# Optimization experiments

Hardware: AMD Instinct MI355X
Metric: run time of the kernel (lower is better)

## Reference

```python
import jax, jax.numpy as jnp
import numpy as np
from jax import lax

G = 16            # graphs in batch
N0 = 2048         # total nodes (128 per graph)
IN_CH = 64
HID = 128
KS = (103, 83)    # ceil(0.8*128), ceil(0.8*103): per-graph nodes kept by each ASAPooling
NEG_SLOPE = 0.2   # ASAPooling leaky_relu slope


def _masked_col_max(M, x, chunk=4):
    # out[i, c] = max_{j : M[j, i]} x[j, c]  (scatter-max over incoming edges), feature-chunked
    N, C = x.shape
    xr = x.T.reshape(C // chunk, chunk, N)
    @jax.checkpoint
    def f(xc):  # [chunk, N_j]
        v = jnp.where(M[None, :, :], xc[:, :, None], -1e30)  # [chunk, j, i]
        return v.max(axis=1)
    return lax.map(f, xr).reshape(C, N).T


def _graph_conv(x, A, w_rel, b_rel, w_root):
    # PyG GraphConv(aggr='mean'): lin_rel(mean_j w_ji * x_j) + lin_root(x); A[src,dst]
    deg = jnp.maximum((A != 0).sum(0).astype(x.dtype), 1.0)  # incoming edge count
    agg = (A.T @ x) / deg[:, None]
    return agg @ w_rel.T + b_rel + x @ w_root.T


def _gpool(x):  # global_mean_pool over equal-sized contiguous graphs
    return x.reshape(G, -1, x.shape[-1]).mean(axis=1)


def _asap_pool(x, A, k, lin_w, lin_b, att_w, att_b, le1_w, le1_b, le2_w, le3_w, le3_b):
    N, C = x.shape
    one = jnp.asarray(1.0, x.dtype)
    A = jnp.where(jnp.eye(N, dtype=bool), one, A)  # add_remaining_self_loops(fill=1)
    M = A != 0
    Mf = M.astype(x.dtype)
    # master query: max over incoming neighbors, then Linear
    q = _masked_col_max(M, x) @ lin_w.T + lin_b                     # [N, C]
    a_q, a_x = att_w[:C], att_w[C:]                                 # att(cat([x_q_i, x_j]))
    logits = jax.nn.leaky_relu((x @ a_x)[:, None] + (q @ a_q)[None, :] + att_b, NEG_SLOPE)  # [j, i]
    S = jnp.where(M, jax.nn.softmax(jnp.where(M, logits, -1e30), axis=0), 0.0)
    x_new = S.T @ x                                                  # cluster reps
    # fitness = sigmoid(LEConv(x_new)): lin3(x_i) + sum_j (lin1(x_j) - lin2(x_i)) over edges
    deg = Mf.sum(0)
    a = x_new @ le1_w + le1_b
    b = x_new @ le2_w
    fitness = jax.nn.sigmoid(Mf.T @ a - deg * b + x_new @ le3_w + le3_b)  # [N]
    n_cur = N // G
    idx = lax.top_k(fitness.reshape(G, n_cur), k)[1]                 # per-graph top-k
    perm = (idx + jnp.arange(G)[:, None] * n_cur).reshape(-1)        # [G*k], grouped by graph
    x_out = x_new[perm] * fitness[perm][:, None]
    S_sel = S[:, perm]                                               # [N, K]
    A2 = S_sel.T @ (A @ S_sel)                                       # S^T A S coarsening
    A2 = jnp.where(jnp.eye(G * k, dtype=bool), one, A2)              # fill_diag(1)
    return x_out, A2


def _forward(x, edge_index, c0_wrel, c0_brel, c0_wroot, cw_rel, cb_rel, cw_root,
             p_lin_w, p_lin_b, p_att_w, p_att_b, p_le1_w, p_le1_b, p_le2_w,
             p_le3_w, p_le3_b, lin1_w, lin1_b, lin2_w, lin2_b):
    A = jnp.zeros((N0, N0), x.dtype).at[edge_index[0], edge_index[1]].add(1.0)
    h = jax.nn.relu(_graph_conv(x, A, c0_wrel, c0_brel, c0_wroot))
    xs = [_gpool(h)]
    p = 0
    for i in range(4):  # num_layers - 1 convs
        h = jax.nn.relu(_graph_conv(h, A, cw_rel[i], cb_rel[i], cw_root[i]))
        xs.append(_gpool(h))
        if i % 2 == 0 and i < 3:
            h, A = _asap_pool(h, A, KS[p], p_lin_w[p], p_lin_b[p], p_att_w[p], p_att_b[p],
                              p_le1_w[p], p_le1_b[p], p_le2_w[p], p_le3_w[p], p_le3_b[p])
            p += 1
    j = jnp.concatenate(xs, axis=-1)                                  # JK 'cat': [G, 5*HID]
    z = jax.nn.relu(j @ lin1_w.T + lin1_b)                            # dropout: eval mode (identity)
    z = z @ lin2_w.T + lin2_b
    return jax.nn.log_softmax(z, axis=-1)


def setup_inputs() -> dict:
    key = jax.random.key(0)
    rng = np.random.default_rng(0)
    n, deg = N0 // G, 16
    sc = rng.random((G, n, n))
    sc[:, np.arange(n), np.arange(n)] = -1.0  # no self loops
    dst = np.argsort(-sc, axis=-1)[:, :, :deg]  # 16 distinct neighbors per node
    src = np.broadcast_to(np.arange(n)[None, :, None], dst.shape)
    off = (np.arange(G) * n)[:, None, None]
    edge_index = jnp.asarray(np.stack([(src + off).ravel(), (dst + off).ravel()]), dtype=jnp.int32)
    ks = jax.random.split(key, 16)
    def lin(k, shape, fan_in):
        return jax.random.normal(k, shape, jnp.float32) / np.sqrt(fan_in)
    return dict(
        x=jax.random.normal(ks[0], (N0, IN_CH), jnp.float32),
        edge_index=edge_index,
        c0_wrel=lin(ks[1], (HID, IN_CH), IN_CH),
        c0_brel=jnp.zeros((HID,), jnp.float32),
        c0_wroot=lin(ks[2], (HID, IN_CH), IN_CH),
        cw_rel=lin(ks[3], (4, HID, HID), HID),
        cb_rel=jnp.zeros((4, HID), jnp.float32),
        cw_root=lin(ks[4], (4, HID, HID), HID),
        p_lin_w=lin(ks[5], (2, HID, HID), HID),
        p_lin_b=jnp.zeros((2, HID), jnp.float32),
        p_att_w=lin(ks[6], (2, 2 * HID), 2 * HID),
        p_att_b=jnp.zeros((2,), jnp.float32),
        p_le1_w=lin(ks[7], (2, HID), HID),
        p_le1_b=jnp.zeros((2,), jnp.float32),
        p_le2_w=lin(ks[8], (2, HID), HID),
        p_le3_w=lin(ks[9], (2, HID), HID),
        p_le3_b=jnp.zeros((2,), jnp.float32),
        lin1_w=lin(ks[10], (HID, 5 * HID), 5 * HID),
        lin1_b=jnp.zeros((HID,), jnp.float32),
        lin2_w=lin(ks[11], (2, HID), HID),
        lin2_b=jnp.zeros((2,), jnp.float32),
    )


def reference(x, edge_index, c0_wrel, c0_brel, c0_wroot, cw_rel, cb_rel, cw_root,
              p_lin_w, p_lin_b, p_att_w, p_att_b, p_le1_w, p_le1_b, p_le2_w,
              p_le3_w, p_le3_b, lin1_w, lin1_b, lin2_w, lin2_b):
    return _forward(x, edge_index, c0_wrel, c0_brel, c0_wroot, cw_rel, cb_rel, cw_root,
                    p_lin_w, p_lin_b, p_att_w, p_att_b, p_le1_w, p_le1_b, p_le2_w,
                    p_le3_w, p_le3_b, lin1_w, lin1_b, lin2_w, lin2_b)
```

## Files before the change

kernel.cpp:

```cpp
#include <hip/hip_runtime.h>

#define NEG_SLOPE 0.2f
typedef unsigned int u32;

__global__ __launch_bounds__(256) void k_build(const int* __restrict__ ei,
                                               u32* __restrict__ Mb,
                                               u32* __restrict__ Rb, int E)
{
    int e = blockIdx.x * 256 + threadIdx.x;
    if (e >= E) return;
    int s = ei[e], d = ei[E + e];
    int g = s >> 7, ls = s & 127, ld = d & 127;
    atomicOr(&Mb[(g * 128 + ld) * 4 + (ls >> 5)], 1u << (ls & 31));
    atomicOr(&Rb[(g * 128 + ls) * 4 + (ld >> 5)], 1u << (ld & 31));
}

__global__ __launch_bounds__(128) void k_prep(
    const float* __restrict__ lin_w, const float* __restrict__ lin_b,
    const float* __restrict__ att_w,
    float* __restrict__ v_out, float* __restrict__ c0_out)
{
    const int p = blockIdx.x;
    const float* lw = lin_w + p * 16384;
    const float* lb = lin_b + p * 128;
    const float* aw = att_w + p * 256;
    const int c = threadIdx.x;
    float s = 0.f;
    for (int c2 = 0; c2 < 128; ++c2) s += aw[c2] * lw[c2 * 128 + c];
    v_out[p * 128 + c] = s;
    if (c < 64) {
        float s0 = aw[c] * lb[c] + aw[c + 64] * lb[c + 64];
        for (int off = 32; off; off >>= 1) s0 += __shfl_xor(s0, off);
        if (c == 0) c0_out[p] = s0;
    }
}

__global__ __launch_bounds__(512) void k_agg_mask(
    const float* __restrict__ h, const u32* __restrict__ Mb,
    float* __restrict__ agg, int n, int Cin)
{
    const int g = blockIdx.x;
    const int q4 = Cin >> 2;
    int idx = blockIdx.y * 512 + threadIdx.x;
    if (idx >= n * q4) return;
    int j = idx / q4, c4 = (idx - j * q4) << 2;
    const u32* m = Mb + (g * 128 + j) * 4;
    u32 m0 = m[0], m1 = m[1], m2 = m[2], m3 = m[3];
    float dv = fmaxf((float)(__popc(m0) + __popc(m1) + __popc(m2) + __popc(m3)), 1.0f);
    const float* hg = h + (size_t)g * n * Cin + c4;
    float sx = 0.f, sy = 0.f, sz = 0.f, sw = 0.f;
    u32 wds[4] = { m0, m1, m2, m3 };
    #pragma unroll
    for (int ww = 0; ww < 4; ++ww) {
        u32 u = wds[ww];
        while (u) {
            int i = (ww << 5) + __ffs(u) - 1; u &= u - 1u;
            float4 hv = *(const float4*)(hg + (size_t)i * Cin);
            sx += hv.x; sy += hv.y; sz += hv.z; sw += hv.w;
        }
    }
    float4 o; o.x = sx / dv; o.y = sy / dv; o.z = sz / dv; o.w = sw / dv;
    *(float4*)(agg + ((size_t)g * n + j) * Cin + c4) = o;
}

__global__ __launch_bounds__(512) void k_agg_dense(
    const float* __restrict__ h, const float* __restrict__ AT,
    const u32* __restrict__ Mb, float* __restrict__ agg, int n)
{
    const int C = 128;
    const int g = blockIdx.x;
    int idx = blockIdx.y * 512 + threadIdx.x;
    if (idx >= n * 32) return;
    int j = idx >> 5, c4 = (idx & 31) << 2;
    const u32* m = Mb + (g * 128 + j) * 4;
    float dv = fmaxf((float)(__popc(m[0]) + __popc(m[1]) + __popc(m[2]) + __popc(m[3])), 1.0f);
    const float* Aj = AT + ((size_t)g * n + j) * n;
    const float* hg = h + (size_t)g * n * C + c4;
    float sx = 0.f, sy = 0.f, sz = 0.f, sw = 0.f;
    for (int i = 0; i < n; ++i) {
        float a = Aj[i];
        float4 hv = *(const float4*)(hg + (size_t)i * C);
        sx += a * hv.x; sy += a * hv.y; sz += a * hv.z; sw += a * hv.w;
    }
    float4 o; o.x = sx / dv; o.y = sy / dv; o.z = sz / dv; o.w = sw / dv;
    *(float4*)(agg + ((size_t)g * n + j) * C + c4) = o;
}

template<int CIN>
__global__ __launch_bounds__(512) void k_out(
    const float* __restrict__ h, const float* __restrict__ agg,
    const float* __restrict__ wrel, const float* __restrict__ brel,
    const float* __restrict__ wroot,
    float* __restrict__ h_out, float* __restrict__ xs,
    int n)
{
    constexpr int L = CIN >> 1;
    constexpr int G = 512 / L;
    constexpr int HALF = L >> 1;
    const int g = blockIdx.x;
    const int gg = threadIdx.x / L;
    const int l  = threadIdx.x % L;
    const int jg = blockIdx.y * G + gg;
    __shared__ float tile[G * 128];

    if (jg < n) {
        const float* xsrc = (l < HALF)
            ? (agg + ((size_t)g * n + jg) * CIN + (l << 2))
            : (h   + ((size_t)g * n + jg) * CIN + ((l - HALF) << 2));
        const float4 xv = *(const float4*)xsrc;
        const float* wbase = (l < HALF) ? (wrel + (l << 2))
                                        : (wroot + ((l - HALF) << 2));
        for (int c2 = 0; c2 < 128; c2 += 4) {
            float4 w0 = *(const float4*)(wbase + (size_t)(c2 + 0) * CIN);
            float4 w1 = *(const float4*)(wbase + (size_t)(c2 + 1) * CIN);
            float4 w2 = *(const float4*)(wbase + (size_t)(c2 + 2) * CIN);
            float4 w3 = *(const float4*)(wbase + (size_t)(c2 + 3) * CIN);
            float a0 = xv.x * w0.x + xv.y * w0.y + xv.z * w0.z + xv.w * w0.w;
            float a1 = xv.x * w1.x + xv.y * w1.y + xv.z * w1.z + xv.w * w1.w;
            float a2 = xv.x * w2.x + xv.y * w2.y + xv.z * w2.z + xv.w * w2.w;
            float a3 = xv.x * w3.x + xv.y * w3.y + xv.z * w3.z + xv.w * w3.w;
            #pragma unroll
            for (int off = L >> 1; off; off >>= 1) {
                a0 += __shfl_xor(a0, off, L);
                a1 += __shfl_xor(a1, off, L);
                a2 += __shfl_xor(a2, off, L);
                a3 += __shfl_xor(a3, off, L);
            }
            if (l == 0) {
                tile[gg * 128 + c2 + 0] = fmaxf(a0 + brel[c2 + 0], 0.0f);
                tile[gg * 128 + c2 + 1] = fmaxf(a1 + brel[c2 + 1], 0.0f);
                tile[gg * 128 + c2 + 2] = fmaxf(a2 + brel[c2 + 2], 0.0f);
                tile[gg * 128 + c2 + 3] = fmaxf(a3 + brel[c2 + 3], 0.0f);
            }
        }
    } else {
        for (int c2 = l; c2 < 128; c2 += L) tile[gg * 128 + c2] = 0.0f;
    }
    __syncthreads();

    const int tid = threadIdx.x;
    for (int idx = tid; idx < G * 32; idx += 512) {
        int r = idx >> 5, c4 = (idx & 31) << 2;
        int j2 = blockIdx.y * G + r;
        if (j2 < n)
            *(float4*)(h_out + ((size_t)g * n + j2) * 128 + c4) =
                *(const float4*)(tile + r * 128 + c4);
    }
    if (tid < 128) {
        float s = 0.f;
        #pragma unroll
        for (int r = 0; r < G; ++r) s += tile[r * 128 + tid];
        atomicAdd(&xs[g * 128 + tid], s / (float)n);
    }
}

__global__ __launch_bounds__(512) void k_attn(
    const float* __restrict__ h, const u32* __restrict__ Mb_g,
    const float* __restrict__ v_g, const float* __restrict__ c0_g,
    const float* __restrict__ att_w,
    float* __restrict__ qa_g, float* __restrict__ xa_g, int n)
{
    const int g = blockIdx.x;
    const int tid = threadIdx.x;
    const int hw = tid >> 5, ln = tid & 31;
    const float* hg = h + (size_t)g * n * 128;
    const int j = blockIdx.y * 16 + hw;
    if (j < n) {
        u32 m[4];
        m[0] = Mb_g[(g * 128 + j) * 4 + 0]; m[1] = Mb_g[(g * 128 + j) * 4 + 1];
        m[2] = Mb_g[(g * 128 + j) * 4 + 2]; m[3] = Mb_g[(g * 128 + j) * 4 + 3];
        m[j >> 5] |= 1u << (j & 31);
        float4 mx = make_float4(-1e30f, -1e30f, -1e30f, -1e30f);
        #pragma unroll
        for (int ww = 0; ww < 4; ++ww) {
            u32 u = m[ww];
            while (u) {
                int i = (ww << 5) + __ffs(u) - 1; u &= u - 1u;
                float4 hv = *(const float4*)(hg + (size_t)i * 128 + ln * 4);
                mx.x = fmaxf(mx.x, hv.x); mx.y = fmaxf(mx.y, hv.y);
                mx.z = fmaxf(mx.z, hv.z); mx.w = fmaxf(mx.w, hv.w);
            }
        }
        float4 vv = *(const float4*)(v_g + ln * 4);
        float acc = mx.x * vv.x + mx.y * vv.y + mx.z * vv.z + mx.w * vv.w;
        #pragma unroll
        for (int off = 16; off; off >>= 1) acc += __shfl_xor(acc, off, 32);
        if (ln == 0) qa_g[g * 128 + j] = acc + c0_g[0];
    }
    const int i = blockIdx.y * 16 + hw;
    if (i < n) {
        float4 hv = *(const float4*)(hg + (size_t)i * 128 + ln * 4);
        float4 aw = *(const float4*)(att_w + 128 + ln * 4);
        float s = hv.x * aw.x + hv.y * aw.y + hv.z * aw.z + hv.w * aw.w;
        #pragma unroll
        for (int off = 16; off; off >>= 1) s += __shfl_xor(s, off, 32);
        if (ln == 0) xa_g[g * 128 + i] = s;
    }
}

__global__ __launch_bounds__(512) void k_soft(
    const u32* __restrict__ Mb_g, const float* __restrict__ qa_g,
    const float* __restrict__ xa_g, const float* __restrict__ att_bp,
    float* __restrict__ S_cm, int n)
{
    const int g = blockIdx.x;
    const int tid = threadIdx.x, lane = tid & 63, wid = tid >> 6;
    const int j = blockIdx.y * 8 + wid;
    if (j >= n) return;
    const float att_b = att_bp[0];
    u32 m[4];
    m[0] = Mb_g[(g * 128 + j) * 4 + 0]; m[1] = Mb_g[(g * 128 + j) * 4 + 1];
    m[2] = Mb_g[(g * 128 + j) * 4 + 2]; m[3] = Mb_g[(g * 128 + j) * 4 + 3];
    m[j >> 5] |= 1u << (j & 31);
    const float qaj = qa_g[g * 128 + j];
    const int i0 = lane, i1 = lane + 64;
    const bool b0 = (i0 < n) && ((m[i0 >> 5] >> (i0 & 31)) & 1u);
    const bool b1 = (i1 < n) && ((m[i1 >> 5] >> (i1 & 31)) & 1u);
    float l0 = -1e30f, l1 = -1e30f;
    if (b0) { float t = xa_g[g * 128 + i0] + qaj + att_b; l0 = (t >= 0.f) ? t : NEG_SLOPE * t; }
    if (b1) { float t = xa_g[g * 128 + i1] + qaj + att_b; l1 = (t >= 0.f) ? t : NEG_SLOPE * t; }
    float mm = fmaxf(l0, l1);
    for (int off = 32; off; off >>= 1) mm = fmaxf(mm, __shfl_xor(mm, off));
    float e0 = b0 ? expf(l0 - mm) : 0.f;
    float e1 = b1 ? expf(l1 - mm) : 0.f;
    float s = e0 + e1;
    for (int off = 32; off; off >>= 1) s += __shfl_xor(s, off);
    float* Sj = S_cm + ((size_t)g * 128 + j) * 128;
    if (i0 < n) Sj[i0] = e0 / s;
    if (i1 < n) Sj[i1] = e1 / s;
}

__global__ __launch_bounds__(512) void k_xnew(
    const float* __restrict__ S_cm, const float* __restrict__ h,
    float* __restrict__ xn, int n)
{
    const int g = blockIdx.x;
    int idx = blockIdx.y * 512 + threadIdx.x;
    if (idx >= n * 32) return;
    int j = idx >> 5, c4 = (idx & 31) << 2;
    const float* Sj = S_cm + ((size_t)g * 128 + j) * 128;
    const float* hg = h + (size_t)g * n * 128 + c4;
    float sx = 0.f, sy = 0.f, sz = 0.f, sw = 0.f;
    for (int i = 0; i < n; ++i) {
        float sv = Sj[i];
        float4 hv = *(const float4*)(hg + (size_t)i * 128);
        sx += sv * hv.x; sy += sv * hv.y; sz += sv * hv.z; sw += sv * hv.w;
    }
    float4 o; o.x = sx; o.y = sy; o.z = sz; o.w = sw;
    *(float4*)(xn + ((size_t)g * 128 + j) * 128 + c4) = o;
}

__global__ __launch_bounds__(512) void k_fit(
    const float* __restrict__ xn, const u32* __restrict__ Mb_g,
    const float* __restrict__ S_cm,
    const float* __restrict__ le1_w, const float* __restrict__ le1_bp,
    const float* __restrict__ le2_w, const float* __restrict__ le3_w,
    const float* __restrict__ le3_bp,
    float* __restrict__ h_out, float* __restrict__ Sselr, float* __restrict__ SselrT,
    int n, int k, int kpad)
{
    const int g = blockIdx.x;
    const float* xg = xn + (size_t)g * 128 * 128;
    __shared__ float a_s[128], b_s[128], c3_s[128], fit_s[128];
    __shared__ int perm_s[128];
    const int tid = threadIdx.x, lane = tid & 63, wid = tid >> 6;

    for (int j = wid; j < n; j += 8) {
        float x0 = xg[j * 128 + lane], x1 = xg[j * 128 + 64 + lane];
        float s1 = x0 * le1_w[lane] + x1 * le1_w[64 + lane];
        float s2 = x0 * le2_w[lane] + x1 * le2_w[64 + lane];
        float s3 = x0 * le3_w[lane] + x1 * le3_w[64 + lane];
        for (int off = 32; off; off >>= 1) {
            s1 += __shfl_xor(s1, off);
            s2 += __shfl_xor(s2, off);
            s3 += __shfl_xor(s3, off);
        }
        if (lane == 0) { a_s[j] = s1 + le1_bp[0]; b_s[j] = s2; c3_s[j] = s3; }
    }
    __syncthreads();
    for (int j = tid; j < n; j += 512) {
        u32 m[4];
        m[0] = Mb_g[(g * 128 + j) * 4 + 0]; m[1] = Mb_g[(g * 128 + j) * 4 + 1];
        m[2] = Mb_g[(g * 128 + j) * 4 + 2]; m[3] = Mb_g[(g * 128 + j) * 4 + 3];
        m[j >> 5] |= 1u << (j & 31);
        float dv = (float)(__popc(m[0]) + __popc(m[1]) + __popc(m[2]) + __popc(m[3]));
        float s = 0.f;
        #pragma unroll
        for (int ww = 0; ww < 4; ++ww) {
            u32 u = m[ww];
            while (u) { int i = (ww << 5) + __ffs(u) - 1; u &= u - 1u; s += a_s[i]; }
        }
        float f = s - dv * b_s[j] + c3_s[j] + le3_bp[0];
        fit_s[j] = 1.0f / (1.0f + expf(-f));
    }
    __syncthreads();
    for (int j = tid; j < n; j += 512) {
        float fj = fit_s[j];
        int r = 0;
        for (int j2 = 0; j2 < n; ++j2) {
            float f2 = fit_s[j2];
            if (f2 > fj || (f2 == fj && j2 < j)) ++r;
        }
        if (r < k) perm_s[r] = j;
    }
    __syncthreads();
    for (int idx = tid; idx < k * 32; idx += 512) {
        int r = idx >> 5, c4 = (idx & 31) << 2;
        int p = perm_s[r]; float f = fit_s[p];
        float4 v = *(const float4*)(xg + p * 128 + c4);
        v.x *= f; v.y *= f; v.z *= f; v.w *= f;
        *(float4*)(h_out + ((size_t)g * k + r) * 128 + c4) = v;
    }
    for (int idx = tid; idx < k * 32; idx += 512) {
        int r = idx >> 5, c4 = (idx & 31) << 2;
        float4 v = *(const float4*)(S_cm + ((size_t)g * 128 + perm_s[r]) * 128 + c4);
        *(float4*)(SselrT + ((size_t)g * 128 + r) * 128 + c4) = v;
    }
    for (int idx = tid; idx < k * n; idx += 512) {
        int cc = idx / n, i = idx - cc * n;
        Sselr[((size_t)g * 128 + i) * kpad + cc] =
            S_cm[((size_t)g * 128 + perm_s[cc]) * 128 + i];
    }
}

__global__ __launch_bounds__(512) void k_T_mask(
    const u32* __restrict__ Rb, const float* __restrict__ Sselr,
    float* __restrict__ T, int n, int k, int kpad)
{
    const int g = blockIdx.x;
    const int ccq = (k + 3) >> 2;
    int idx = blockIdx.y * 512 + threadIdx.x;
    if (idx >= n * ccq) return;
    int i = idx / ccq, c4 = (idx - i * ccq) << 2;
    u32 m[4];
    m[0] = Rb[(g * 128 + i) * 4 + 0]; m[1] = Rb[(g * 128 + i) * 4 + 1];
    m[2] = Rb[(g * 128 + i) * 4 + 2]; m[3] = Rb[(g * 128 + i) * 4 + 3];
    m[i >> 5] |= 1u << (i & 31);
    float sx = 0.f, sy = 0.f, sz = 0.f, sw = 0.f;
    #pragma unroll
    for (int ww = 0; ww < 4; ++ww) {
        u32 u = m[ww];
        while (u) {
            int j = (ww << 5) + __ffs(u) - 1; u &= u - 1u;
            float4 v = *(const float4*)(Sselr + ((size_t)g * 128 + j) * kpad + c4);
            sx += v.x; sy += v.y; sz += v.z; sw += v.w;
        }
    }
    float4 o; o.x = sx; o.y = sy; o.z = sz; o.w = sw;
    *(float4*)(T + ((size_t)g * 128 + i) * kpad + c4) = o;
}

__global__ __launch_bounds__(512) void k_T_dense(
    const float* __restrict__ A, const float* __restrict__ Sselr,
    float* __restrict__ T, int n, int k, int kpad)
{
    const int g = blockIdx.x;
    const int ccq = (k + 3) >> 2;
    int idx = blockIdx.y * 512 + threadIdx.x;
    if (idx >= n * ccq) return;
    int i = idx / ccq, c4 = (idx - i * ccq) << 2;
    const float* Ai = A + ((size_t)g * n + i) * n;
    float sx = 0.f, sy = 0.f, sz = 0.f, sw = 0.f;
    for (int j = 0; j < n; ++j) {
        float a = Ai[j];
        float4 v = *(const float4*)(Sselr + ((size_t)g * 128 + j) * kpad + c4);
        sx += a * v.x; sy += a * v.y; sz += a * v.z; sw += a * v.w;
    }
    float4 o; o.x = sx; o.y = sy; o.z = sz; o.w = sw;
    *(float4*)(T + ((size_t)g * 128 + i) * kpad + c4) = o;
}

__global__ __launch_bounds__(512) void k_A2(
    const float* __restrict__ SselrT, const float* __restrict__ T,
    float* __restrict__ A_out, float* __restrict__ AT_out,
    u32* __restrict__ Mb_out, int n, int k, int kpad)
{
    const int g = blockIdx.x;
    int idx = blockIdx.y * 512 + threadIdx.x;
    if (idx >= k * k) return;
    int r = idx / k, cc = idx - r * k;
    const float* Sr = SselrT + ((size_t)g * 128 + r) * 128;
    const float* Tg = T + (size_t)g * 128 * kpad;
    float s = 0.f;
    for (int i = 0; i < n; ++i) s += Sr[i] * Tg[i * kpad + cc];
    float val = (r == cc) ? 1.0f : s;
    A_out[((size_t)g * k + r) * k + cc] = val;
    AT_out[((size_t)g * k + cc) * k + r] = val;
    if (val != 0.0f)
        atomicOr(&Mb_out[((size_t)g * 128 + cc) * 4 + (r >> 5)], 1u << (r & 31));
}

__global__ __launch_bounds__(256) void k_final(
    const float* __restrict__ xs,
    const float* __restrict__ w1, const float* __restrict__ b1,
    const float* __restrict__ w2, const float* __restrict__ b2,
    float* __restrict__ out)
{
    const int g = blockIdx.x;
    __shared__ float j_s[640];
    __shared__ float z1[128];
    const int tid = threadIdx.x, lane = tid & 63, wid = tid >> 6;

    for (int idx = tid; idx < 640; idx += 256) {
        int t = idx >> 7, c = idx & 127;
        j_s[idx] = xs[t * 2048 + g * 128 + c];
    }
    __syncthreads();
    for (int c2 = wid; c2 < 128; c2 += 4) {
        const float* wrow = w1 + (size_t)c2 * 640;
        float s = 0.f;
        #pragma unroll
        for (int it = 0; it < 10; ++it) {
            int kk = it * 64 + lane;
            s += j_s[kk] * wrow[kk];
        }
        for (int off = 32; off; off >>= 1) s += __shfl_xor(s, off);
        if (lane == 0) z1[c2] = fmaxf(s + b1[c2], 0.0f);
    }
    __syncthreads();
    if (wid == 0) {
        float zv0 = z1[lane], zv1 = z1[lane + 64];
        float za = zv0 * w2[lane] + zv1 * w2[lane + 64];
        float zb = zv0 * w2[128 + lane] + zv1 * w2[192 + lane];
        for (int off = 32; off; off >>= 1) {
            za += __shfl_xor(za, off);
            zb += __shfl_xor(zb, off);
        }
        if (lane == 0) {
            za += b2[0]; zb += b2[1];
            float m = fmaxf(za, zb);
            float lse = m + logf(expf(za - m) + expf(zb - m));
            out[g * 2 + 0] = za - lse;
            out[g * 2 + 1] = zb - lse;
        }
    }
}

extern "C" void kernel_launch(void* const* d_in, const int* in_sizes, int n_in,
                              void* d_out, int out_size, void* d_ws, size_t ws_size,
                              hipStream_t stream)
{
    (void)n_in; (void)out_size; (void)ws_size;
    const float* x        = (const float*)d_in[0];
    const int*   ei       = (const int*)  d_in[1];
    const float* c0_wrel  = (const float*)d_in[2];
    const float* c0_brel  = (const float*)d_in[3];
    const float* c0_wroot = (const float*)d_in[4];
    const float* cw_rel   = (const float*)d_in[5];
    const float* cb_rel   = (const float*)d_in[6];
    const float* cw_root  = (const float*)d_in[7];
    const float* p_lin_w  = (const float*)d_in[8];
    const float* p_lin_b  = (const float*)d_in[9];
    const float* p_att_w  = (const float*)d_in[10];
    const float* p_att_b  = (const float*)d_in[11];
    const float* p_le1_w  = (const float*)d_in[12];
    const float* p_le1_b  = (const float*)d_in[13];
    const float* p_le2_w  = (const float*)d_in[14];
    const float* p_le3_w  = (const float*)d_in[15];
    const float* p_le3_b  = (const float*)d_in[16];
    const float* lin1_w   = (const float*)d_in[17];
    const float* lin1_b   = (const float*)d_in[18];
    const float* lin2_w   = (const float*)d_in[19];
    const float* lin2_b   = (const float*)d_in[20];
    float* out = (float*)d_out;

    const int E = in_sizes[1] / 2;

    u32*   Mb1 = (u32*)d_ws;
    u32*   Rb1 = Mb1 + 8192;
    float* xsf = (float*)(Rb1 + 8192);
    u32*   Mb2 = (u32*)(xsf + 10240);
    u32*   Mb3 = Mb2 + 8192;
    float* qaw = (float*)(Mb3 + 8192);
    float* xaw = qaw + 2048;
    float* vbuf = xaw + 2048;
    float* c0buf = vbuf + 256;
    float* agg = c0buf + 4;
    float* hA  = agg + 262144;
    float* hB  = hA  + 262144;
    float* Scm = hB  + 262144;
    float* xnw = Scm + 262144;
    float* Ssr = xnw + 262144;
    float* SsT = Ssr + 229376;
    float* A2  = SsT + 262144;
    float* A2T = A2  + 169744;
    float* A3  = A2T + 169744;
    float* A3T = A3  + 110224;
    float* Tw  = agg;

    hipMemsetAsync(d_ws, 0, (8192 + 8192 + 10240 + 8192 + 8192) * 4, stream);
    k_build<<<(E + 255) / 256, 256, 0, stream>>>(ei, Mb1, Rb1, E);
    k_prep<<<2, 128, 0, stream>>>(p_lin_w, p_lin_b, p_att_w, vbuf, c0buf);

    k_agg_mask<<<dim3(16, 4), 512, 0, stream>>>(x, Mb1, agg, 128, 64);
    k_out<64><<<dim3(16, 8), 512, 0, stream>>>(x, agg, c0_wrel, c0_brel, c0_wroot,
                                               hA, xsf + 0 * 2048, 128);
    k_agg_mask<<<dim3(16, 8), 512, 0, stream>>>(hA, Mb1, agg, 128, 128);
    k_out<128><<<dim3(16, 16), 512, 0, stream>>>(hA, agg, cw_rel, cb_rel, cw_root,
                                                 hB, xsf + 1 * 2048, 128);
    k_attn<<<dim3(16, 8), 512, 0, stream>>>(hB, Mb1, vbuf, c0buf, p_att_w, qaw, xaw, 128);
    k_soft<<<dim3(16, 16), 512, 0, stream>>>(Mb1, qaw, xaw, p_att_b, Scm, 128);
    k_xnew<<<dim3(16, 8), 512, 0, stream>>>(Scm, hB, xnw, 128);
    k_fit<<<16, 512, 0, stream>>>(xnw, Mb1, Scm,
                                  p_le1_w, p_le1_b, p_le2_w, p_le3_w, p_le3_b,
                                  hA, Ssr, SsT, 128, 103, 112);
    k_T_mask<<<dim3(16, 7), 512, 0, stream>>>(Rb1, Ssr, Tw, 128, 103, 112);
    k_A2<<<dim3(16, 21), 512, 0, stream>>>(SsT, Tw, A2, A2T, Mb2, 128, 103, 112);
    k_agg_dense<<<dim3(16, 7), 512, 0, stream>>>(hA, A2T, Mb2, agg, 103);
    k_out<128><<<dim3(16, 13), 512, 0, stream>>>(hA, agg, cw_rel + 16384, cb_rel + 128,
                                                 cw_root + 16384, hB, xsf + 2 * 2048, 103);
    k_agg_dense<<<dim3(16, 7), 512, 0, stream>>>(hB, A2T, Mb2, agg, 103);
    k_out<128><<<dim3(16, 13), 512, 0, stream>>>(hB, agg, cw_rel + 2 * 16384, cb_rel + 2 * 128,
                                                 cw_root + 2 * 16384, hA, xsf + 3 * 2048, 103);
    k_attn<<<dim3(16, 7), 512, 0, stream>>>(hA, Mb2, vbuf + 128, c0buf + 1,
                                            p_att_w + 256, qaw, xaw, 103);
    k_soft<<<dim3(16, 13), 512, 0, stream>>>(Mb2, qaw, xaw, p_att_b + 1, Scm, 103);
    k_xnew<<<dim3(16, 7), 512, 0, stream>>>(Scm, hA, xnw, 103);
    k_fit<<<16, 512, 0, stream>>>(xnw, Mb2, Scm,
                                  p_le1_w + 128, p_le1_b + 1, p_le2_w + 128,
                                  p_le3_w + 128, p_le3_b + 1,
                                  hB, Ssr, SsT, 103, 83, 96);
    k_T_dense<<<dim3(16, 5), 512, 0, stream>>>(A2, Ssr, Tw, 103, 83, 96);
    k_A2<<<dim3(16, 14), 512, 0, stream>>>(SsT, Tw, A3, A3T, Mb3, 103, 83, 96);
    k_agg_dense<<<dim3(16, 6), 512, 0, stream>>>(hB, A3T, Mb3, agg, 83);
    k_out<128><<<dim3(16, 11), 512, 0, stream>>>(hB, agg, cw_rel + 3 * 16384, cb_rel + 3 * 128,
                                                 cw_root + 3 * 16384, hA, xsf + 4 * 2048, 83);

    k_final<<<16, 256, 0, stream>>>(xsf, lin1_w, lin1_b, lin2_w, lin2_b, out);
}
```

Measured before the change: 555.2 us.

## Fuse neighbor aggregation into GraphConv output kernel

```diff
diff --git a/kernel.cpp b/kernel.cpp
--- a/kernel.cpp
+++ b/kernel.cpp
@@ -35,60 +35,10 @@
     }
 }
 
-__global__ __launch_bounds__(512) void k_agg_mask(
+template<int CIN, bool DENSE>
+__global__ __launch_bounds__(512) void k_conv(
     const float* __restrict__ h, const u32* __restrict__ Mb,
-    float* __restrict__ agg, int n, int Cin)
-{
-    const int g = blockIdx.x;
-    const int q4 = Cin >> 2;
-    int idx = blockIdx.y * 512 + threadIdx.x;
-    if (idx >= n * q4) return;
-    int j = idx / q4, c4 = (idx - j * q4) << 2;
-    const u32* m = Mb + (g * 128 + j) * 4;
-    u32 m0 = m[0], m1 = m[1], m2 = m[2], m3 = m[3];
-    float dv = fmaxf((float)(__popc(m0) + __popc(m1) + __popc(m2) + __popc(m3)), 1.0f);
-    const float* hg = h + (size_t)g * n * Cin + c4;
-    float sx = 0.f, sy = 0.f, sz = 0.f, sw = 0.f;
-    u32 wds[4] = { m0, m1, m2, m3 };
-    #pragma unroll
-    for (int ww = 0; ww < 4; ++ww) {
-        u32 u = wds[ww];
-        while (u) {
-            int i = (ww << 5) + __ffs(u) - 1; u &= u - 1u;
-            float4 hv = *(const float4*)(hg + (size_t)i * Cin);
-            sx += hv.x; sy += hv.y; sz += hv.z; sw += hv.w;
-        }
-    }
-    float4 o; o.x = sx / dv; o.y = sy / dv; o.z = sz / dv; o.w = sw / dv;
-    *(float4*)(agg + ((size_t)g * n + j) * Cin + c4) = o;
-}
-
-__global__ __launch_bounds__(512) void k_agg_dense(
-    const float* __restrict__ h, const float* __restrict__ AT,
-    const u32* __restrict__ Mb, float* __restrict__ agg, int n)
-{
-    const int C = 128;
-    const int g = blockIdx.x;
-    int idx = blockIdx.y * 512 + threadIdx.x;
-    if (idx >= n * 32) return;
-    int j = idx >> 5, c4 = (idx & 31) << 2;
-    const u32* m = Mb + (g * 128 + j) * 4;
-    float dv = fmaxf((float)(__popc(m[0]) + __popc(m[1]) + __popc(m[2]) + __popc(m[3])), 1.0f);
-    const float* Aj = AT + ((size_t)g * n + j) * n;
-    const float* hg = h + (size_t)g * n * C + c4;
-    float sx = 0.f, sy = 0.f, sz = 0.f, sw = 0.f;
-    for (int i = 0; i < n; ++i) {
-        float a = Aj[i];
-        float4 hv = *(const float4*)(hg + (size_t)i * C);
-        sx += a * hv.x; sy += a * hv.y; sz += a * hv.z; sw += a * hv.w;
-    }
-    float4 o; o.x = sx / dv; o.y = sy / dv; o.z = sz / dv; o.w = sw / dv;
-    *(float4*)(agg + ((size_t)g * n + j) * C + c4) = o;
-}
-
-template<int CIN>
-__global__ __launch_bounds__(512) void k_out(
-    const float* __restrict__ h, const float* __restrict__ agg,
+    const float* __restrict__ AT,
     const float* __restrict__ wrel, const float* __restrict__ brel,
     const float* __restrict__ wroot,
     float* __restrict__ h_out, float* __restrict__ xs,
@@ -104,10 +54,54 @@
     __shared__ float tile[G * 128];
 
     if (jg < n) {
-        const float* xsrc = (l < HALF)
-            ? (agg + ((size_t)g * n + jg) * CIN + (l << 2))
-            : (h   + ((size_t)g * n + jg) * CIN + ((l - HALF) << 2));
-        const float4 xv = *(const float4*)xsrc;
+        const int slot = l & (HALF - 1);
+        const int c4 = slot << 2;
+        const float* hsrc = h + (size_t)g * n * CIN;
+        const u32* mp = Mb + (g * 128 + jg) * 4;
+        u32 m0 = mp[0], m1 = mp[1], m2 = mp[2], m3 = mp[3];
+        float dv = fmaxf((float)(__popc(m0) + __popc(m1) + __popc(m2) + __popc(m3)), 1.0f);
+        float4 acc = make_float4(0.f, 0.f, 0.f, 0.f);
+        const float* hc = hsrc + c4;
+        if constexpr (!DENSE) {
+            u32 wa = (l < HALF) ? m0 : m2;
+            u32 wb = (l < HALF) ? m1 : m3;
+            const int ba = (l < HALF) ? 0 : 64;
+            u32 u = wa;
+            while (u) {
+                int i = ba + __ffs(u) - 1; u &= u - 1u;
+                float4 v = *(const float4*)(hc + (size_t)i * CIN);
+                acc.x += v.x; acc.y += v.y; acc.z += v.z; acc.w += v.w;
+            }
+            u = wb;
+            while (u) {
+                int i = ba + 32 + __ffs(u) - 1; u &= u - 1u;
+                float4 v = *(const float4*)(hc + (size_t)i * CIN);
+                acc.x += v.x; acc.y += v.y; acc.z += v.z; acc.w += v.w;
+            }
+        } else {
+            const float* Aj = AT + ((size_t)g * n + jg) * n;
+            const int ibeg = (l < HALF) ? 0 : (n >> 1);
+            const int iend = (l < HALF) ? (n >> 1) : n;
+            for (int i = ibeg; i < iend; ++i) {
+                float a = Aj[i];
+                float4 v = *(const float4*)(hc + (size_t)i * CIN);
+                acc.x += a * v.x; acc.y += a * v.y;
+                acc.z += a * v.z; acc.w += a * v.w;
+            }
+        }
+        acc.x += __shfl_xor(acc.x, HALF, L);
+        acc.y += __shfl_xor(acc.y, HALF, L);
+        acc.z += __shfl_xor(acc.z, HALF, L);
+        acc.w += __shfl_xor(acc.w, HALF, L);
+
+        float4 xv;
+        if (l < HALF) {
+            xv.x = acc.x / dv; xv.y = acc.y / dv;
+            xv.z = acc.z / dv; xv.w = acc.w / dv;
+        } else {
+            xv = *(const float4*)(hsrc + (size_t)jg * CIN + c4);
+        }
+
         const float* wbase = (l < HALF) ? (wrel + (l << 2))
                                         : (wroot + ((l - HALF) << 2));
         for (int c2 = 0; c2 < 128; c2 += 4) {
@@ -492,12 +486,10 @@
     k_build<<<(E + 255) / 256, 256, 0, stream>>>(ei, Mb1, Rb1, E);
     k_prep<<<2, 128, 0, stream>>>(p_lin_w, p_lin_b, p_att_w, vbuf, c0buf);
 
-    k_agg_mask<<<dim3(16, 4), 512, 0, stream>>>(x, Mb1, agg, 128, 64);
-    k_out<64><<<dim3(16, 8), 512, 0, stream>>>(x, agg, c0_wrel, c0_brel, c0_wroot,
-                                               hA, xsf + 0 * 2048, 128);
-    k_agg_mask<<<dim3(16, 8), 512, 0, stream>>>(hA, Mb1, agg, 128, 128);
-    k_out<128><<<dim3(16, 16), 512, 0, stream>>>(hA, agg, cw_rel, cb_rel, cw_root,
-                                                 hB, xsf + 1 * 2048, 128);
+    k_conv<64, false><<<dim3(16, 8), 512, 0, stream>>>(
+        x, Mb1, nullptr, c0_wrel, c0_brel, c0_wroot, hA, xsf + 0 * 2048, 128);
+    k_conv<128, false><<<dim3(16, 16), 512, 0, stream>>>(
+        hA, Mb1, nullptr, cw_rel, cb_rel, cw_root, hB, xsf + 1 * 2048, 128);
     k_attn<<<dim3(16, 8), 512, 0, stream>>>(hB, Mb1, vbuf, c0buf, p_att_w, qaw, xaw, 128);
     k_soft<<<dim3(16, 16), 512, 0, stream>>>(Mb1, qaw, xaw, p_att_b, Scm, 128);
     k_xnew<<<dim3(16, 8), 512, 0, stream>>>(Scm, hB, xnw, 128);
@@ -506,12 +498,12 @@
                                   hA, Ssr, SsT, 128, 103, 112);
     k_T_mask<<<dim3(16, 7), 512, 0, stream>>>(Rb1, Ssr, Tw, 128, 103, 112);
     k_A2<<<dim3(16, 21), 512, 0, stream>>>(SsT, Tw, A2, A2T, Mb2, 128, 103, 112);
-    k_agg_dense<<<dim3(16, 7), 512, 0, stream>>>(hA, A2T, Mb2, agg, 103);
-    k_out<128><<<dim3(16, 13), 512, 0, stream>>>(hA, agg, cw_rel + 16384, cb_rel + 128,
-                                                 cw_root + 16384, hB, xsf + 2 * 2048, 103);
-    k_agg_dense<<<dim3(16, 7), 512, 0, stream>>>(hB, A2T, Mb2, agg, 103);
-    k_out<128><<<dim3(16, 13), 512, 0, stream>>>(hB, agg, cw_rel + 2 * 16384, cb_rel + 2 * 128,
-                                                 cw_root + 2 * 16384, hA, xsf + 3 * 2048, 103);
+    k_conv<128, true><<<dim3(16, 13), 512, 0, stream>>>(
+        hA, Mb2, A2T, cw_rel + 16384, cb_rel + 128, cw_root + 16384,
+        hB, xsf + 2 * 2048, 103);
+    k_conv<128, true><<<dim3(16, 13), 512, 0, stream>>>(
+        hB, Mb2, A2T, cw_rel + 2 * 16384, cb_rel + 2 * 128, cw_root + 2 * 16384,
+        hA, xsf + 3 * 2048, 103);
     k_attn<<<dim3(16, 7), 512, 0, stream>>>(hA, Mb2, vbuf + 128, c0buf + 1,
                                             p_att_w + 256, qaw, xaw, 103);
     k_soft<<<dim3(16, 13), 512, 0, stream>>>(Mb2, qaw, xaw, p_att_b + 1, Scm, 103);
@@ -522,9 +514,9 @@
                                   hB, Ssr, SsT, 103, 83, 96);
     k_T_dense<<<dim3(16, 5), 512, 0, stream>>>(A2, Ssr, Tw, 103, 83, 96);
     k_A2<<<dim3(16, 14), 512, 0, stream>>>(SsT, Tw, A3, A3T, Mb3, 103, 83, 96);
-    k_agg_dense<<<dim3(16, 6), 512, 0, stream>>>(hB, A3T, Mb3, agg, 83);
-    k_out<128><<<dim3(16, 11), 512, 0, stream>>>(hB, agg, cw_rel + 3 * 16384, cb_rel + 3 * 128,
-                                                 cw_root + 3 * 16384, hA, xsf + 4 * 2048, 83);
+    k_conv<128, true><<<dim3(16, 11), 512, 0, stream>>>(
+        hB, Mb3, A3T, cw_rel + 3 * 16384, cb_rel + 3 * 128, cw_root + 3 * 16384,
+        hA, xsf + 4 * 2048, 83);
 
     k_final<<<16, 256, 0, stream>>>(xsf, lin1_w, lin1_b, lin2_w, lin2_b, out);
 }
```

After: 514.2 us. 7.4% less time.
